# Performance work log

Measured on AMD Instinct MI355X. Metric: run time of the kernel, lower is better.

The kernel has to match this reference:

```python
import jax, jax.numpy as jnp
import numpy as np

N_NODES = 100000   # B*A = 4 * 25000 nodes after the reshape in forward()
N_EDGES = 1600000  # avg degree 16
F_IN = 2           # node_features
HID = 64           # hidden_size
K = 3              # diffusion order (hardcoded in RecurrentGCN)


def _glorot(key, shape):
    fan_in, fan_out = shape[-2], shape[-1]
    s = float(np.sqrt(6.0 / (fan_in + fan_out)))
    return jax.random.uniform(key, shape, jnp.float32, -s, s)


def setup_inputs() -> dict:
    key = jax.random.key(0)
    ks = jax.random.split(key, 12)
    x = jax.random.normal(ks[0], (4, 25000, 12, F_IN), dtype=jnp.float32)
    edge_index = jax.random.randint(ks[1], (2, N_EDGES), 0, N_NODES, dtype=jnp.int32)
    edge_weight = jax.random.uniform(ks[2], (N_EDGES,), dtype=jnp.float32)

    def cell(k, cin):
        kw = jax.random.split(k, 3)
        # 3 gates (z, r, h), each a DConv with weight [2, K, cin, HID]
        W = jnp.stack([_glorot(kw[i], (2, K, cin, HID)) for i in range(3)])
        b = jnp.zeros((3, HID), dtype=jnp.float32)
        return W, b

    enc1_W, enc1_b = cell(ks[3], F_IN + HID)
    enc2_W, enc2_b = cell(ks[4], HID + HID)
    dec1_W, dec1_b = cell(ks[5], F_IN + HID)
    dec2_W, dec2_b = cell(ks[6], HID + HID)
    lin_W = _glorot(ks[7], (HID, F_IN))
    lin_b = jnp.zeros((F_IN,), dtype=jnp.float32)
    return dict(x=x, edge_index=edge_index, edge_weight=edge_weight,
                enc1_W=enc1_W, enc1_b=enc1_b, enc2_W=enc2_W, enc2_b=enc2_b,
                dec1_W=dec1_W, dec1_b=dec1_b, dec2_W=dec2_W, dec2_b=dec2_b,
                lin_W=lin_W, lin_b=lin_b)


def _dconv(v, src, dst, do_inv, di_inv, W, b):
    # Dual-direction diffusion conv (DConv, torch_geometric_temporal), order K.
    # Normalization is applied at the node level before gather so the
    # edge-level multiply (E x C) never needs to be a stored residual.
    def pout(u):  # out[dst] += deg_out_inv[src] * u[src]
        return jax.ops.segment_sum((do_inv[:, None] * u)[src], dst, num_segments=N_NODES)

    def pin(u):   # out[src] += deg_in_inv[dst] * u[dst]
        return jax.ops.segment_sum((di_inv[:, None] * u)[dst], src, num_segments=N_NODES)

    H = v @ (W[0, 0] + W[1, 0])
    t1o, t1i = pout(v), pin(v)
    H = H + t1o @ W[0, 1] + t1i @ W[1, 1]
    t0o = t0i = v
    for k in range(2, K):  # Chebyshev-style recurrence
        t2o = 2.0 * pout(t1o) - t0o
        t2i = 2.0 * pin(t1i) - t0i
        H = H + t2o @ W[0, k] + t2i @ W[1, k]
        t0o, t1o = t1o, t2o
        t0i, t1i = t1i, t2i
    return H + b


def _dcrnn(x, h, src, dst, do_inv, di_inv, W, b):
    # GRU cell whose gates are diffusion convolutions over [x, h].
    xh = jnp.concatenate([x, h], axis=1)
    Z = jax.nn.sigmoid(_dconv(xh, src, dst, do_inv, di_inv, W[0], b[0]))
    R = jax.nn.sigmoid(_dconv(xh, src, dst, do_inv, di_inv, W[1], b[1]))
    Ht = jnp.tanh(_dconv(jnp.concatenate([x, R * h], axis=1),
                         src, dst, do_inv, di_inv, W[2], b[2]))
    return Z * h + (1.0 - Z) * Ht


def _forward(x, edge_index, edge_weight,
             enc1_W, enc1_b, enc2_W, enc2_b,
             dec1_W, dec1_b, dec2_W, dec2_b, lin_W, lin_b):
    B, A, S, Fd = x.shape
    # permute(0,1,3,2) then [..., 0] == x[:, :, 0, :]; flatten to [B*A, F]
    xs = x[:, :, 0, :].reshape(B * A, Fd)
    src, dst = edge_index[0], edge_index[1]
    deg_out = jax.ops.segment_sum(edge_weight, src, num_segments=N_NODES)
    deg_in = jax.ops.segment_sum(edge_weight, dst, num_segments=N_NODES)
    do_inv = jnp.where(deg_out > 0, 1.0 / deg_out, 0.0)
    di_inv = jnp.where(deg_in > 0, 1.0 / deg_in, 0.0)
    zeros = jnp.zeros((B * A, HID), dtype=x.dtype)
    h_enc1 = _dcrnn(xs, zeros, src, dst, do_inv, di_inv, enc1_W, enc1_b)
    h = jax.nn.relu(h_enc1)
    h_enc2 = _dcrnn(h, zeros, src, dst, do_inv, di_inv, enc2_W, enc2_b)
    h = _dcrnn(xs, h_enc1, src, dst, do_inv, di_inv, dec1_W, dec1_b)
    h = jax.nn.relu(h)
    h = _dcrnn(h, h_enc2, src, dst, do_inv, di_inv, dec2_W, dec2_b)
    return h @ lin_W + lin_b


def reference(x, edge_index, edge_weight,
              enc1_W, enc1_b, enc2_W, enc2_b,
              dec1_W, dec1_b, dec2_W, dec2_b, lin_W, lin_b):
    return _forward(x, edge_index, edge_weight,
                    enc1_W, enc1_b, enc2_W, enc2_b,
                    dec1_W, dec1_b, dec2_W, dec2_b, lin_W, lin_b)
```

## Files before the change

kernel.cpp:

```cpp
#include <hip/hip_runtime.h>

#define N_NODES 100000
#define N_EDGES 1600000

typedef _Float16 f16;
typedef _Float16 f16x8 __attribute__((ext_vector_type(8)));
typedef float f32x4 __attribute__((ext_vector_type(4)));

__device__ __forceinline__ float sigf(float x) { return 1.f / (1.f + __expf(-x)); }


__global__ void count_kernel(const int* __restrict__ src, const int* __restrict__ dst,
                             int* __restrict__ cntO, int* __restrict__ cntI,
                             int* __restrict__ slotO, int* __restrict__ slotI)
{
    int i = blockIdx.x * 256 + threadIdx.x;
    if (i >= N_EDGES) return;
    slotO[i] = atomicAdd(&cntO[dst[i]], 1);
    slotI[i] = atomicAdd(&cntI[src[i]], 1);
}

__global__ __launch_bounds__(1024) void scan2_kernel(const int* __restrict__ cntA, int* __restrict__ rpA,
                                                     const int* __restrict__ cntB, int* __restrict__ rpB,
                                                     int n)
{
    const int* cnt = blockIdx.x ? cntB : cntA;
    int* rp = blockIdx.x ? rpB : rpA;
    __shared__ int wsum[16];
    __shared__ int carry;
    int tid = threadIdx.x, lane = tid & 63, wid = tid >> 6;
    if (tid == 0) { rp[0] = 0; carry = 0; }
    __syncthreads();
    for (int base = 0; base < n; base += 1024) {
        int idx = base + tid;
        int x = (idx < n) ? cnt[idx] : 0;
        #pragma unroll
        for (int off = 1; off < 64; off <<= 1) {
            int y = __shfl_up(x, off);
            if (lane >= off) x += y;
        }
        if (lane == 63) wsum[wid] = x;
        __syncthreads();
        if (wid == 0 && lane < 16) {
            int y = wsum[lane];
            #pragma unroll
            for (int off = 1; off < 16; off <<= 1) {
                int z = __shfl_up(y, off);
                if (lane >= off) y += z;
            }
            wsum[lane] = y;
        }
        __syncthreads();
        int tot = x + (wid ? wsum[wid - 1] : 0) + carry;
        if (idx < n) rp[idx + 1] = tot;
        __syncthreads();
        if (tid == 1023) carry = tot;
        __syncthreads();
    }
}

__global__ void fill_kernel(const int* __restrict__ src, const int* __restrict__ dst,
                            const float* __restrict__ ew,
                            const int* __restrict__ rpO, const int* __restrict__ rpI,
                            const int* __restrict__ slotO, const int* __restrict__ slotI,
                            int2* __restrict__ adj2O, int2* __restrict__ adj2I)
{
    int i = blockIdx.x * 256 + threadIdx.x;
    if (i >= N_EDGES) return;
    int s = src[i], d = dst[i];
    int wb = __float_as_int(ew[i]);
    int2 eo; eo.x = s; eo.y = wb;
    adj2O[rpO[d] + slotO[i]] = eo;
    int2 ei; ei.x = d; ei.y = wb;
    adj2I[rpI[s] + slotI[i]] = ei;
}

__global__ void finalize_kernel(const int* __restrict__ rpO, const int2* __restrict__ adj2O,
                                int* __restrict__ adjO, float* __restrict__ di_inv,
                                const int* __restrict__ rpI, const int2* __restrict__ adj2I,
                                int* __restrict__ adjI, float* __restrict__ do_inv)
{
    int n = blockIdx.x * 256 + threadIdx.x;
    if (n >= N_NODES) return;
    float s = 0.f;
    for (int e = rpO[n]; e < rpO[n + 1]; ++e) {
        int2 v = adj2O[e];
        adjO[e] = v.x;
        s += __int_as_float(v.y);
    }
    di_inv[n] = (s > 0.f) ? 1.f / s : 0.f;
    float t = 0.f;
    for (int e = rpI[n]; e < rpI[n + 1]; ++e) {
        int2 v = adj2I[e];
        adjI[e] = v.x;
        t += __int_as_float(v.y);
    }
    do_inv[n] = (t > 0.f) ? 1.f / t : 0.f;
}

__global__ void prep_w(const float* __restrict__ W, int C, int SA, int PWA, int rA,
                       int gLo, int gHi, int COLS, int XS, f16* __restrict__ outw)
{
    int total = (SA + XS) * COLS * 32;
    int idx = blockIdx.x * 256 + threadIdx.x;
    if (idx >= total) return;
    int k32 = idx & 31;
    int c = (idx >> 5) % COLS;
    int s = (idx >> 5) / COLS;
    int g = (c < 64 || gHi < 0) ? gLo : gHi;
    int col = (c >= 64) ? c - 64 : c;
    int p, r;
    if (s < SA) { p = s / PWA; r = rA + (s % PWA) * 32 + k32; }
    else {
        if (k32 < 10) { p = k32 >> 1; r = k32 & 1; }
        else { outw[idx] = (f16)0.f; return; }
    }
    auto wv = [&](int d, int k) {
        return W[((((size_t)(g * 2 + d) * 3 + k) * C + r) << 6) + col];
    };
    float val;
    if (p == 0)      val = wv(0, 0) + wv(1, 0) - wv(0, 2) - wv(1, 2);
    else if (p == 1) val = wv(0, 1);
    else if (p == 2) val = 2.f * wv(0, 2);
    else if (p == 3) val = wv(1, 1);
    else             val = 2.f * wv(1, 2);
    outw[idx] = (f16)val;
}

__global__ void prep_enc1w(const float* __restrict__ W, float* __restrict__ outw)
{
    int idx = blockIdx.x * 256 + threadIdx.x;
    if (idx >= 1280) return;
    int c = idx & 127, k = idx >> 7;
    int g = (c < 64) ? 0 : 2, col = c & 63;
    int p = k >> 1, r = k & 1;
    const int C = 66;
    auto wv = [&](int d, int kk) {
        return W[((((size_t)(g * 2 + d) * 3 + kk) * C + r) << 6) + col];
    };
    float val;
    if (p == 0)      val = wv(0, 0) + wv(1, 0) - wv(0, 2) - wv(1, 2);
    else if (p == 1) val = wv(0, 1);
    else if (p == 2) val = 2.f * wv(0, 2);
    else if (p == 3) val = wv(1, 1);
    else             val = 2.f * wv(1, 2);
    outw[idx] = val;
}

__global__ void xcat_init(const float* __restrict__ x, f16* __restrict__ xcat)
{
    int i = blockIdx.x * 256 + threadIdx.x;
    if (i >= N_NODES * 32) return;
    int n = i >> 5, c = i & 31;
    float v = (c < 2) ? x[(size_t)n * 24 + c] : 0.f;
    xcat[i] = (f16)v;
}

__global__ void prop2d_kernel(const int* __restrict__ rpA, const int* __restrict__ adjA,
                              const float* __restrict__ scA, int cinA, int coutA,
                              const int* __restrict__ rpB, const int* __restrict__ adjB,
                              const float* __restrict__ scB, int cinB, int coutB,
                              f16* __restrict__ xcat)
{
    const int* rp; const int* adj; const float* sc; int cin, cout;
    if (blockIdx.y == 0) { rp = rpA; adj = adjA; sc = scA; cin = cinA; cout = coutA; }
    else                 { rp = rpB; adj = adjB; sc = scB; cin = cinB; cout = coutB; }
    int n = blockIdx.x * 256 + threadIdx.x;
    if (n >= N_NODES) return;
    int beg = rp[n], end = rp[n + 1];
    float a0 = 0.f, a1 = 0.f;
    for (int e = beg; e < end; ++e) {
        int s = adj[e];
        float w = sc[s];
        a0 += w * (float)xcat[((size_t)s << 5) + cin];
        a1 += w * (float)xcat[((size_t)s << 5) + cin + 1];
    }
    xcat[((size_t)n << 5) + cout] = (f16)a0;
    xcat[((size_t)n << 5) + cout + 1] = (f16)a1;
}

template <int LPN>
__global__ __launch_bounds__(256) void propk(
    const int* __restrict__ rpA, const int* __restrict__ adjA, const float* __restrict__ scA,
    const f16* __restrict__ uA, f16* __restrict__ oA,
    const int* __restrict__ rpB, const int* __restrict__ adjB, const float* __restrict__ scB,
    const f16* __restrict__ uB, f16* __restrict__ oB,
    int ldu, int ldo)
{
    const int* RP; const int* ADJ; const float* SC; const f16* U; f16* OUT;
    if (blockIdx.y == 0) { RP = rpA; ADJ = adjA; SC = scA; U = uA; OUT = oA; }
    else                 { RP = rpB; ADJ = adjB; SC = scB; U = uB; OUT = oB; }
    constexpr int NPB = 256 / LPN;
    int node = blockIdx.x * NPB + (threadIdx.x / LPN);
    int l = threadIdx.x % LPN;
    if (node >= N_NODES) return;
    int b = RP[node], e = RP[node + 1];
    float a[8] = {0.f, 0.f, 0.f, 0.f, 0.f, 0.f, 0.f, 0.f};
    float c[8] = {0.f, 0.f, 0.f, 0.f, 0.f, 0.f, 0.f, 0.f};
    int i = b;
    for (; i + 1 < e; i += 2) {
        int s0 = ADJ[i], s1 = ADJ[i + 1];
        float w0 = SC[s0], w1 = SC[s1];
        f16x8 u0 = *(const f16x8*)(U + (size_t)s0 * ldu + (l << 3));
        f16x8 u1 = *(const f16x8*)(U + (size_t)s1 * ldu + (l << 3));
        #pragma unroll
        for (int j = 0; j < 8; ++j) { a[j] += w0 * (float)u0[j]; c[j] += w1 * (float)u1[j]; }
    }
    if (i < e) {
        int s = ADJ[i];
        float w = SC[s];
        f16x8 u0 = *(const f16x8*)(U + (size_t)s * ldu + (l << 3));
        #pragma unroll
        for (int j = 0; j < 8; ++j) a[j] += w * (float)u0[j];
    }
    f16x8 r;
    #pragma unroll
    for (int j = 0; j < 8; ++j) r[j] = (f16)(a[j] + c[j]);
    *(f16x8*)(OUT + (size_t)node * ldo + (l << 3)) = r;
}

template <int SA, int XS, int COLS, int ACT>
__global__ __launch_bounds__(256) void mfma_gemm(
    const f16* __restrict__ uA, const f16* __restrict__ tA0, const f16* __restrict__ tA1,
    const f16* __restrict__ tA2, const f16* __restrict__ tA3,
    int lAu, int cAu, int lAt, int cAt,
    const f16* __restrict__ xcat, const f16* __restrict__ wstep,
    const f16* __restrict__ addX,
    const float* __restrict__ biasLo, const float* __restrict__ biasHi,
    f16* __restrict__ out, int os,
    const f16* __restrict__ hmul, int hs,
    f16* __restrict__ out2, const f16* __restrict__ zin)
{
    __shared__ f16 As[64][40];
    __shared__ f16 Ws[COLS][40];
    const int row0 = blockIdx.x * 64;
    const int tid = threadIdx.x;
    const int wave = tid >> 6, lane = tid & 63;
    const int lr = lane & 15, lk = lane >> 4;
    const int ka = lk << 3;
    constexpr int RT = (COLS == 128) ? 4 : 2;
    constexpr int PWA = SA / 5;
    constexpr int STEPS = SA + XS;
    f32x4 acc[RT][2] = {};
    const f16* tA[4] = { tA0, tA1, tA2, tA3 };

    #pragma unroll
    for (int s = 0; s < STEPS; ++s) {
        __syncthreads();
        {
            int r = tid >> 2, seg = tid & 3;
            int grow = row0 + r;
            const f16* srcp;
            if (s < SA) {
                int p = s / PWA, ch = s % PWA;
                const f16* base = (p == 0) ? uA : tA[p - 1];
                int ld = (p == 0) ? lAu : lAt;
                int co = (p == 0) ? cAu : cAt;
                srcp = base + (size_t)grow * ld + co + ch * 32 + (seg << 3);
            } else {
                srcp = xcat + (((size_t)grow) << 5) + (seg << 3);
            }
            int4 v = (grow < N_NODES) ? *(const int4*)srcp : make_int4(0, 0, 0, 0);
            *(int4*)&As[r][seg << 3] = v;
        }
        for (int q = tid; q < COLS * 4; q += 256) {
            int c = q >> 2, seg = q & 3;
            *(int4*)&Ws[c][seg << 3] =
                *(const int4*)(wstep + (((size_t)(s * COLS + c)) << 5) + (seg << 3));
        }
        __syncthreads();
        if (COLS == 128) {
            f16x8 b0 = *(const f16x8*)&Ws[wave * 32 + lr][ka];
            f16x8 b1 = *(const f16x8*)&Ws[wave * 32 + 16 + lr][ka];
            #pragma unroll
            for (int rt = 0; rt < RT; ++rt) {
                f16x8 a = *(const f16x8*)&As[rt * 16 + lr][ka];
                acc[rt][0] = __builtin_amdgcn_mfma_f32_16x16x32_f16(a, b0, acc[rt][0], 0, 0, 0);
                acc[rt][1] = __builtin_amdgcn_mfma_f32_16x16x32_f16(a, b1, acc[rt][1], 0, 0, 0);
            }
        } else {
            f16x8 b0 = *(const f16x8*)&Ws[(wave & 1) * 32 + lr][ka];
            f16x8 b1 = *(const f16x8*)&Ws[(wave & 1) * 32 + 16 + lr][ka];
            #pragma unroll
            for (int rt = 0; rt < RT; ++rt) {
                f16x8 a = *(const f16x8*)&As[(wave >> 1) * 32 + rt * 16 + lr][ka];
                acc[rt][0] = __builtin_amdgcn_mfma_f32_16x16x32_f16(a, b0, acc[rt][0], 0, 0, 0);
                acc[rt][1] = __builtin_amdgcn_mfma_f32_16x16x32_f16(a, b1, acc[rt][1], 0, 0, 0);
            }
        }
    }
    if constexpr (ACT == 4) {
        __shared__ float zbuf[64][65];
        float treg[RT][2][4];
        #pragma unroll
        for (int rt = 0; rt < RT; ++rt)
            #pragma unroll
            for (int ct = 0; ct < 2; ++ct) {
                int col = wave * 32 + ct * 16 + lr;
                #pragma unroll
                for (int j = 0; j < 4; ++j) {
                    int r = rt * 16 + lk * 4 + j;
                    float v = acc[rt][ct][j] + ((col < 64) ? biasLo[col] : biasHi[col - 64]);
                    if (col < 64) zbuf[r][col] = sigf(v);
                    else          treg[rt][ct][j] = tanhf(v);
                }
            }
        __syncthreads();
        #pragma unroll
        for (int rt = 0; rt < RT; ++rt)
            #pragma unroll
            for (int ct = 0; ct < 2; ++ct) {
                int col = wave * 32 + ct * 16 + lr;
                if (col < 64) continue;
                #pragma unroll
                for (int j = 0; j < 4; ++j) {
                    int r = rt * 16 + lk * 4 + j;
                    int grow = row0 + r;
                    if (grow >= N_NODES) continue;
                    float h = (1.f - zbuf[r][col - 64]) * treg[rt][ct][j];
                    out[(size_t)grow * os + (col - 64)] = (f16)h;
                }
            }
    } else if constexpr (ACT == 5) {
        #pragma unroll
        for (int rt = 0; rt < RT; ++rt)
            #pragma unroll
            for (int ct = 0; ct < 2; ++ct) {
                int col = wave * 32 + ct * 16 + lr;
                #pragma unroll
                for (int j = 0; j < 4; ++j) {
                    int grow = row0 + rt * 16 + lk * 4 + j;
                    if (grow >= N_NODES) continue;
                    float v = acc[rt][ct][j] + ((col < 64) ? biasLo[col] : biasHi[col - 64]);
                    float sg = sigf(v);
                    if (col < 64)
                        out[((size_t)grow << 6) + col] = (f16)sg;
                    else
                        out2[((size_t)grow << 6) + (col - 64)] =
                            (f16)(sg * (float)hmul[(size_t)grow * hs + (col - 64)]);
                }
            }
    } else {
        #pragma unroll
        for (int rt = 0; rt < RT; ++rt) {
            int rbase = (COLS == 128) ? rt * 16 : (wave >> 1) * 32 + rt * 16;
            #pragma unroll
            for (int ct = 0; ct < 2; ++ct) {
                int col = ((COLS == 128) ? wave * 32 : (wave & 1) * 32) + ct * 16 + lr;
                #pragma unroll
                for (int j = 0; j < 4; ++j) {
                    int grow = row0 + rbase + lk * 4 + j;
                    if (grow >= N_NODES) continue;
                    float v = acc[rt][ct][j];
                    if (addX)   v += (float)addX[((size_t)grow << 6) + col];
                    if (biasLo) v += (col < 64) ? biasLo[col] : biasHi[col - 64];
                    if (ACT == 2) v = tanhf(v);
                    else if (ACT == 6) {
                        float t = tanhf(v);
                        float z = (float)zin[((size_t)grow << 6) + col];
                        float hv = (float)hmul[(size_t)grow * hs + col];
                        v = fmaxf(z * hv + (1.f - z) * t, 0.f);
                    }
                    out[(size_t)grow * os + col] = (f16)v;
                }
            }
        }
    }
}

__global__ __launch_bounds__(256) void enc1_kernel(const f16* __restrict__ xcat,
                                                   const float* __restrict__ We1,
                                                   const float* __restrict__ b,
                                                   f16* __restrict__ c1)
{
    int node = (blockIdx.x << 2) + (threadIdx.x >> 6);
    int lane = threadIdx.x & 63;
    float az = b[lane], at = b[128 + lane];
    #pragma unroll
    for (int k = 0; k < 10; ++k) {
        float xv = (float)xcat[((size_t)node << 5) + k];
        az += xv * We1[k * 128 + lane];
        at += xv * We1[k * 128 + 64 + lane];
    }
    float z = sigf(az), t = tanhf(at);
    float h = (1.f - z) * t;
    size_t o = (size_t)node * 128 + lane;
    c1[o] = (f16)fmaxf(h, 0.f);
    c1[o + 64] = (f16)h;
}

__global__ __launch_bounds__(256) void final_kernel(const f16* __restrict__ zb, const f16* __restrict__ gT,
                                                    const f16* __restrict__ h2,
                                                    const float* __restrict__ lW, const float* __restrict__ lb,
                                                    float* __restrict__ out)
{
    int node = (blockIdx.x << 2) + (threadIdx.x >> 6);
    int lane = threadIdx.x & 63;
    size_t i = ((size_t)node << 6) + lane;
    float z = (float)zb[i];
    float d = z * (float)h2[(size_t)node * 128 + lane] + (1.f - z) * (float)gT[i];
    float s0 = d * lW[lane * 2];
    float s1 = d * lW[lane * 2 + 1];
    #pragma unroll
    for (int off = 32; off > 0; off >>= 1) {
        s0 += __shfl_down(s0, off);
        s1 += __shfl_down(s1, off);
    }
    if (lane == 0) {
        out[node * 2]     = s0 + lb[0];
        out[node * 2 + 1] = s1 + lb[1];
    }
}


extern "C" void kernel_launch(void* const* d_in, const int* in_sizes, int n_in,
                              void* d_out, int out_size, void* d_ws, size_t ws_size,
                              hipStream_t stream)
{
    (void)in_sizes; (void)n_in; (void)out_size;
    const float* x   = (const float*)d_in[0];
    const int*  eidx = (const int*)d_in[1];
    const float* ew  = (const float*)d_in[2];
    const float* e1W = (const float*)d_in[3];
    const float* e1b = (const float*)d_in[4];
    const float* e2W = (const float*)d_in[5];
    const float* e2b = (const float*)d_in[6];
    const float* d1W = (const float*)d_in[7];
    const float* d1b = (const float*)d_in[8];
    const float* d2W = (const float*)d_in[9];
    const float* d2b = (const float*)d_in[10];
    const float* lW  = (const float*)d_in[11];
    const float* lb  = (const float*)d_in[12];
    const int* src = eidx;
    const int* dst = eidx + N_EDGES;
    const int N = N_NODES, E = N_EDGES;

    char* p = (char*)d_ws;
    auto carve = [&](size_t bytes) { char* r = p; p += (bytes + 255) & ~(size_t)255; return r; };
    size_t NC = (size_t)N * 128 * 2;
    size_t NH = (size_t)N * 64 * 2;
    int*   cntO  = (int*)carve((size_t)2 * N * 4);
    int*   cntI  = cntO + N;
    int*   rpO   = (int*)carve((size_t)(N + 1) * 4);
    int*   rpI   = (int*)carve((size_t)(N + 1) * 4);
    int*   slotO = (int*)carve((size_t)E * 4);
    int*   slotI = (int*)carve((size_t)E * 4);
    char*  uni   = carve((size_t)2 * E * 8);
    int2*  adj2O = (int2*)uni;
    int2*  adj2I = (int2*)(uni + (size_t)E * 8);
    f16*   ct0   = (f16*)uni;
    f16*   ct1   = (f16*)carve(NC);
    f16*   ct2   = (f16*)carve(NC);
    f16*   ct3   = (f16*)carve(NC);
    float* do_inv = (float*)carve((size_t)N * 4);
    float* di_inv = (float*)carve((size_t)N * 4);
    f16*   xcat = (f16*)carve((size_t)N * 32 * 2);
    f16*   c1   = (f16*)carve(NC);
    f16*   c2   = (f16*)carve(NC);
    f16*   g    = (f16*)carve(NH);
    f16*   gT   = (f16*)carve(NH);
    f16*   zb   = (f16*)carve(NH);
    f16* wE2   = (f16*)carve((size_t)10 * 128 * 32 * 2);
    f16* wD1zr = (f16*)carve((size_t)11 * 128 * 32 * 2);
    f16* wD1c  = (f16*)carve((size_t)11 * 64 * 32 * 2);
    f16* wD2zr = (f16*)carve((size_t)20 * 128 * 32 * 2);
    f16* wD2cA = (f16*)carve((size_t)10 * 64 * 32 * 2);
    f16* wD2cB = (f16*)carve((size_t)10 * 64 * 32 * 2);
    float* We1 = (float*)carve((size_t)1280 * 4);

    size_t needed = (size_t)(p - (char*)d_ws);
    if (needed > ws_size) return;

    const int eg = (E + 255) / 256;
    const int ng = (N + 255) / 256;
    const int GB = 25000;

    hipMemsetAsync(cntO, 0, (size_t)2 * N * 4, stream);
    count_kernel<<<eg, 256, 0, stream>>>(src, dst, cntO, cntI, slotO, slotI);
    scan2_kernel<<<2, 1024, 0, stream>>>(cntO, rpO, cntI, rpI, N);
    fill_kernel<<<eg, 256, 0, stream>>>(src, dst, ew, rpO, rpI, slotO, slotI, adj2O, adj2I);
    int* adjO = slotO;
    int* adjI = slotI;
    finalize_kernel<<<ng, 256, 0, stream>>>(rpO, adj2O, adjO, di_inv, rpI, adj2I, adjI, do_inv);

    auto wprep = [&](const float* W, int C, int SA, int PWA, int rA,
                     int gLo, int gHi, int COLS, int XS, f16* o) {
        int total = (SA + XS) * COLS * 32;
        prep_w<<<(total + 255) / 256, 256, 0, stream>>>(W, C, SA, PWA, rA, gLo, gHi, COLS, XS, o);
    };
    wprep(e2W, 128, 10, 2, 0,  0,  2, 128, 0, wE2);
    wprep(d1W, 66,  10, 2, 2,  0,  1, 128, 1, wD1zr);
    wprep(d1W, 66,  10, 2, 2,  2, -1,  64, 1, wD1c);
    wprep(d2W, 128, 20, 4, 0,  0,  1, 128, 0, wD2zr);
    wprep(d2W, 128, 10, 2, 0,  2, -1,  64, 0, wD2cA);
    wprep(d2W, 128, 10, 2, 64, 2, -1,  64, 0, wD2cB);
    prep_enc1w<<<5, 256, 0, stream>>>(e1W, We1);

    xcat_init<<<(N * 32 + 255) / 256, 256, 0, stream>>>(x, xcat);
    dim3 ng2(ng, 2);
    prop2d_kernel<<<ng2, 256, 0, stream>>>(rpO, adjO, do_inv, 0, 2,
                                           rpI, adjI, di_inv, 0, 6, xcat);
    prop2d_kernel<<<ng2, 256, 0, stream>>>(rpO, adjO, do_inv, 2, 4,
                                           rpI, adjI, di_inv, 6, 8, xcat);

    auto props128 = [&](const f16* u) {
        dim3 pg(N / 16, 2);
        propk<16><<<pg, 256, 0, stream>>>(rpO, adjO, do_inv, u, ct0,
                                          rpI, adjI, di_inv, u, ct2, 128, 128);
        propk<16><<<pg, 256, 0, stream>>>(rpO, adjO, do_inv, ct0, ct1,
                                          rpI, adjI, di_inv, ct2, ct3, 128, 128);
    };
    auto props64 = [&](const f16* u) {
        dim3 pg(N / 32, 2);
        propk<8><<<pg, 256, 0, stream>>>(rpO, adjO, do_inv, u, ct0,
                                         rpI, adjI, di_inv, u, ct2, 64, 128);
        propk<8><<<pg, 256, 0, stream>>>(rpO, adjO, do_inv, ct0, ct1,
                                         rpI, adjI, di_inv, ct2, ct3, 128, 128);
    };
    const int gg = (N + 63) / 64;

    enc1_kernel<<<GB, 256, 0, stream>>>(xcat, We1, e1b, c1);
    props128(c1);
    mfma_gemm<10, 0, 128, 4><<<gg, 256, 0, stream>>>(
        c1, ct0, ct1, ct2, ct3, 128, 0, 128, 0, nullptr, wE2,
        nullptr, e2b, e2b + 128, c2 + 64, 128, nullptr, 0, nullptr, nullptr);
    mfma_gemm<10, 1, 128, 5><<<gg, 256, 0, stream>>>(
        c1, ct0, ct1, ct2, ct3, 128, 64, 128, 64, xcat, wD1zr,
        nullptr, d1b, d1b + 64, zb, 64, c1 + 64, 128, g, nullptr);
    props64(g);
    mfma_gemm<10, 1, 64, 6><<<gg, 256, 0, stream>>>(
        g, ct0, ct1, ct2, ct3, 64, 0, 128, 0, xcat, wD1c,
        nullptr, d1b + 128, d1b + 128, c2, 128, c1 + 64, 128, nullptr, zb);
    props128(c2);
    mfma_gemm<20, 0, 128, 5><<<gg, 256, 0, stream>>>(
        c2, ct0, ct1, ct2, ct3, 128, 0, 128, 0, nullptr, wD2zr,
        nullptr, d2b, d2b + 64, zb, 64, c2 + 64, 128, g, nullptr);
    mfma_gemm<10, 0, 64, 0><<<gg, 256, 0, stream>>>(
        c2, ct0, ct1, ct2, ct3, 128, 0, 128, 0, nullptr, wD2cA,
        nullptr, nullptr, nullptr, gT, 64, nullptr, 0, nullptr, nullptr);
    props64(g);
    mfma_gemm<10, 0, 64, 2><<<gg, 256, 0, stream>>>(
        g, ct0, ct1, ct2, ct3, 64, 0, 128, 0, nullptr, wD2cB,
        gT, d2b + 128, d2b + 128, gT, 64, nullptr, 0, nullptr, nullptr);
    final_kernel<<<GB, 256, 0, stream>>>(zb, gT, c2 + 64, lW, lb, (float*)d_out);
}
```

Before: 1.470 ms.

## Pack per-edge normalization into CSR entries and deepen GEMM K-step to 64

```diff
diff --git a/kernel.cpp b/kernel.cpp
--- a/kernel.cpp
+++ b/kernel.cpp
@@ -76,26 +76,27 @@
 }
 
 __global__ void finalize_kernel(const int* __restrict__ rpO, const int2* __restrict__ adj2O,
-                                int* __restrict__ adjO, float* __restrict__ di_inv,
+                                float* __restrict__ di_inv,
                                 const int* __restrict__ rpI, const int2* __restrict__ adj2I,
-                                int* __restrict__ adjI, float* __restrict__ do_inv)
+                                float* __restrict__ do_inv)
 {
     int n = blockIdx.x * 256 + threadIdx.x;
     if (n >= N_NODES) return;
     float s = 0.f;
-    for (int e = rpO[n]; e < rpO[n + 1]; ++e) {
-        int2 v = adj2O[e];
-        adjO[e] = v.x;
-        s += __int_as_float(v.y);
-    }
+    for (int e = rpO[n]; e < rpO[n + 1]; ++e) s += __int_as_float(adj2O[e].y);
     di_inv[n] = (s > 0.f) ? 1.f / s : 0.f;
     float t = 0.f;
-    for (int e = rpI[n]; e < rpI[n + 1]; ++e) {
-        int2 v = adj2I[e];
-        adjI[e] = v.x;
-        t += __int_as_float(v.y);
-    }
+    for (int e = rpI[n]; e < rpI[n + 1]; ++e) t += __int_as_float(adj2I[e].y);
     do_inv[n] = (t > 0.f) ? 1.f / t : 0.f;
+}
+
+__global__ void coeff_kernel(int2* __restrict__ adj2O, const float* __restrict__ do_inv,
+                             int2* __restrict__ adj2I, const float* __restrict__ di_inv)
+{
+    int i = blockIdx.x * 256 + threadIdx.x;
+    if (i >= N_EDGES) return;
+    int2 v = adj2O[i]; v.y = __float_as_int(do_inv[v.x]); adj2O[i] = v;
+    int2 w = adj2I[i]; w.y = __float_as_int(di_inv[w.x]); adj2I[i] = w;
 }
 
 __global__ void prep_w(const float* __restrict__ W, int C, int SA, int PWA, int rA,
@@ -156,24 +157,24 @@
     xcat[i] = (f16)v;
 }
 
-__global__ void prop2d_kernel(const int* __restrict__ rpA, const int* __restrict__ adjA,
-                              const float* __restrict__ scA, int cinA, int coutA,
-                              const int* __restrict__ rpB, const int* __restrict__ adjB,
-                              const float* __restrict__ scB, int cinB, int coutB,
+__global__ void prop2d_kernel(const int* __restrict__ rpA, const int2* __restrict__ adjA,
+                              int cinA, int coutA,
+                              const int* __restrict__ rpB, const int2* __restrict__ adjB,
+                              int cinB, int coutB,
                               f16* __restrict__ xcat)
 {
-    const int* rp; const int* adj; const float* sc; int cin, cout;
-    if (blockIdx.y == 0) { rp = rpA; adj = adjA; sc = scA; cin = cinA; cout = coutA; }
-    else                 { rp = rpB; adj = adjB; sc = scB; cin = cinB; cout = coutB; }
+    const int* rp; const int2* adj; int cin, cout;
+    if (blockIdx.y == 0) { rp = rpA; adj = adjA; cin = cinA; cout = coutA; }
+    else                 { rp = rpB; adj = adjB; cin = cinB; cout = coutB; }
     int n = blockIdx.x * 256 + threadIdx.x;
     if (n >= N_NODES) return;
     int beg = rp[n], end = rp[n + 1];
     float a0 = 0.f, a1 = 0.f;
     for (int e = beg; e < end; ++e) {
-        int s = adj[e];
-        float w = sc[s];
-        a0 += w * (float)xcat[((size_t)s << 5) + cin];
-        a1 += w * (float)xcat[((size_t)s << 5) + cin + 1];
+        int2 v = adj[e];
+        float w = __int_as_float(v.y);
+        a0 += w * (float)xcat[((size_t)v.x << 5) + cin];
+        a1 += w * (float)xcat[((size_t)v.x << 5) + cin + 1];
     }
     xcat[((size_t)n << 5) + cout] = (f16)a0;
     xcat[((size_t)n << 5) + cout + 1] = (f16)a1;
@@ -181,15 +182,15 @@
 
 template <int LPN>
 __global__ __launch_bounds__(256) void propk(
-    const int* __restrict__ rpA, const int* __restrict__ adjA, const float* __restrict__ scA,
+    const int* __restrict__ rpA, const int2* __restrict__ adjA,
     const f16* __restrict__ uA, f16* __restrict__ oA,
-    const int* __restrict__ rpB, const int* __restrict__ adjB, const float* __restrict__ scB,
+    const int* __restrict__ rpB, const int2* __restrict__ adjB,
     const f16* __restrict__ uB, f16* __restrict__ oB,
     int ldu, int ldo)
 {
-    const int* RP; const int* ADJ; const float* SC; const f16* U; f16* OUT;
-    if (blockIdx.y == 0) { RP = rpA; ADJ = adjA; SC = scA; U = uA; OUT = oA; }
-    else                 { RP = rpB; ADJ = adjB; SC = scB; U = uB; OUT = oB; }
+    const int* RP; const int2* ADJ; const f16* U; f16* OUT;
+    if (blockIdx.y == 0) { RP = rpA; ADJ = adjA; U = uA; OUT = oA; }
+    else                 { RP = rpB; ADJ = adjB; U = uB; OUT = oB; }
     constexpr int NPB = 256 / LPN;
     int node = blockIdx.x * NPB + (threadIdx.x / LPN);
     int l = threadIdx.x % LPN;
@@ -199,17 +200,17 @@
     float c[8] = {0.f, 0.f, 0.f, 0.f, 0.f, 0.f, 0.f, 0.f};
     int i = b;
     for (; i + 1 < e; i += 2) {
-        int s0 = ADJ[i], s1 = ADJ[i + 1];
-        float w0 = SC[s0], w1 = SC[s1];
-        f16x8 u0 = *(const f16x8*)(U + (size_t)s0 * ldu + (l << 3));
-        f16x8 u1 = *(const f16x8*)(U + (size_t)s1 * ldu + (l << 3));
+        int2 n0 = ADJ[i], n1 = ADJ[i + 1];
+        float w0 = __int_as_float(n0.y), w1 = __int_as_float(n1.y);
+        f16x8 u0 = *(const f16x8*)(U + (size_t)n0.x * ldu + (l << 3));
+        f16x8 u1 = *(const f16x8*)(U + (size_t)n1.x * ldu + (l << 3));
         #pragma unroll
         for (int j = 0; j < 8; ++j) { a[j] += w0 * (float)u0[j]; c[j] += w1 * (float)u1[j]; }
     }
     if (i < e) {
-        int s = ADJ[i];
-        float w = SC[s];
-        f16x8 u0 = *(const f16x8*)(U + (size_t)s * ldu + (l << 3));
+        int2 n0 = ADJ[i];
+        float w = __int_as_float(n0.y);
+        f16x8 u0 = *(const f16x8*)(U + (size_t)n0.x * ldu + (l << 3));
         #pragma unroll
         for (int j = 0; j < 8; ++j) a[j] += w * (float)u0[j];
     }
@@ -225,14 +226,14 @@
     const f16* __restrict__ tA2, const f16* __restrict__ tA3,
     int lAu, int cAu, int lAt, int cAt,
     const f16* __restrict__ xcat, const f16* __restrict__ wstep,
-    const f16* __restrict__ addX,
+    const f16* __restrict__ addX, int axs,
     const float* __restrict__ biasLo, const float* __restrict__ biasHi,
     f16* __restrict__ out, int os,
     const f16* __restrict__ hmul, int hs,
-    f16* __restrict__ out2, const f16* __restrict__ zin)
-{
-    __shared__ f16 As[64][40];
-    __shared__ f16 Ws[COLS][40];
+    f16* __restrict__ out2, int o2s, const f16* __restrict__ zin)
+{
+    __shared__ f16 As[64][72];
+    __shared__ f16 Ws[COLS][72];
     const int row0 = blockIdx.x * 64;
     const int tid = threadIdx.x;
     const int wave = tid >> 6, lane = tid & 63;
@@ -241,51 +242,62 @@
     constexpr int RT = (COLS == 128) ? 4 : 2;
     constexpr int PWA = SA / 5;
     constexpr int STEPS = SA + XS;
+    constexpr int NIT = (STEPS + 1) / 2;
     f32x4 acc[RT][2] = {};
     const f16* tA[4] = { tA0, tA1, tA2, tA3 };
 
     #pragma unroll
-    for (int s = 0; s < STEPS; ++s) {
-        __syncthreads();
-        {
-            int r = tid >> 2, seg = tid & 3;
-            int grow = row0 + r;
-            const f16* srcp;
-            if (s < SA) {
-                int p = s / PWA, ch = s % PWA;
-                const f16* base = (p == 0) ? uA : tA[p - 1];
-                int ld = (p == 0) ? lAu : lAt;
-                int co = (p == 0) ? cAu : cAt;
-                srcp = base + (size_t)grow * ld + co + ch * 32 + (seg << 3);
+    for (int sp = 0; sp < NIT; ++sp) {
+        const int s0 = sp * 2;
+        const int nsub = (s0 + 2 <= STEPS) ? 2 : 1;
+        __syncthreads();
+        #pragma unroll
+        for (int t = 0; t < nsub; ++t) {
+            int s = s0 + t;
+            {
+                int r = tid >> 2, seg = tid & 3;
+                int grow = row0 + r;
+                const f16* srcp;
+                if (s < SA) {
+                    int pp = s / PWA, ch = s % PWA;
+                    const f16* base = (pp == 0) ? uA : tA[pp - 1];
+                    int ld = (pp == 0) ? lAu : lAt;
+                    int co = (pp == 0) ? cAu : cAt;
+                    srcp = base + (size_t)grow * ld + co + ch * 32 + (seg << 3);
+                } else {
+                    srcp = xcat + (((size_t)grow) << 5) + (seg << 3);
+                }
+                int4 v = (grow < N_NODES) ? *(const int4*)srcp : make_int4(0, 0, 0, 0);
+                *(int4*)&As[r][t * 32 + (seg << 3)] = v;
+            }
+            for (int q = tid; q < COLS * 4; q += 256) {
+                int cc = q >> 2, sg = q & 3;
+                *(int4*)&Ws[cc][t * 32 + (sg << 3)] =
+                    *(const int4*)(wstep + (((size_t)(s * COLS + cc)) << 5) + (sg << 3));
+            }
+        }
+        __syncthreads();
+        #pragma unroll
+        for (int t = 0; t < nsub; ++t) {
+            int kb = t * 32 + ka;
+            if (COLS == 128) {
+                f16x8 b0 = *(const f16x8*)&Ws[wave * 32 + lr][kb];
+                f16x8 b1 = *(const f16x8*)&Ws[wave * 32 + 16 + lr][kb];
+                #pragma unroll
+                for (int rt = 0; rt < RT; ++rt) {
+                    f16x8 a = *(const f16x8*)&As[rt * 16 + lr][kb];
+                    acc[rt][0] = __builtin_amdgcn_mfma_f32_16x16x32_f16(a, b0, acc[rt][0], 0, 0, 0);
+                    acc[rt][1] = __builtin_amdgcn_mfma_f32_16x16x32_f16(a, b1, acc[rt][1], 0, 0, 0);
+                }
             } else {
-                srcp = xcat + (((size_t)grow) << 5) + (seg << 3);
-            }
-            int4 v = (grow < N_NODES) ? *(const int4*)srcp : make_int4(0, 0, 0, 0);
-            *(int4*)&As[r][seg << 3] = v;
-        }
-        for (int q = tid; q < COLS * 4; q += 256) {
-            int c = q >> 2, seg = q & 3;
-            *(int4*)&Ws[c][seg << 3] =
-                *(const int4*)(wstep + (((size_t)(s * COLS + c)) << 5) + (seg << 3));
-        }
-        __syncthreads();
-        if (COLS == 128) {
-            f16x8 b0 = *(const f16x8*)&Ws[wave * 32 + lr][ka];
-            f16x8 b1 = *(const f16x8*)&Ws[wave * 32 + 16 + lr][ka];
-            #pragma unroll
-            for (int rt = 0; rt < RT; ++rt) {
-                f16x8 a = *(const f16x8*)&As[rt * 16 + lr][ka];
-                acc[rt][0] = __builtin_amdgcn_mfma_f32_16x16x32_f16(a, b0, acc[rt][0], 0, 0, 0);
-                acc[rt][1] = __builtin_amdgcn_mfma_f32_16x16x32_f16(a, b1, acc[rt][1], 0, 0, 0);
-            }
-        } else {
-            f16x8 b0 = *(const f16x8*)&Ws[(wave & 1) * 32 + lr][ka];
-            f16x8 b1 = *(const f16x8*)&Ws[(wave & 1) * 32 + 16 + lr][ka];
-            #pragma unroll
-            for (int rt = 0; rt < RT; ++rt) {
-                f16x8 a = *(const f16x8*)&As[(wave >> 1) * 32 + rt * 16 + lr][ka];
-                acc[rt][0] = __builtin_amdgcn_mfma_f32_16x16x32_f16(a, b0, acc[rt][0], 0, 0, 0);
-                acc[rt][1] = __builtin_amdgcn_mfma_f32_16x16x32_f16(a, b1, acc[rt][1], 0, 0, 0);
+                f16x8 b0 = *(const f16x8*)&Ws[(wave & 1) * 32 + lr][kb];
+                f16x8 b1 = *(const f16x8*)&Ws[(wave & 1) * 32 + 16 + lr][kb];
+                #pragma unroll
+                for (int rt = 0; rt < RT; ++rt) {
+                    f16x8 a = *(const f16x8*)&As[(wave >> 1) * 32 + rt * 16 + lr][kb];
+                    acc[rt][0] = __builtin_amdgcn_mfma_f32_16x16x32_f16(a, b0, acc[rt][0], 0, 0, 0);
+                    acc[rt][1] = __builtin_amdgcn_mfma_f32_16x16x32_f16(a, b1, acc[rt][1], 0, 0, 0);
+                }
             }
         }
     }
@@ -334,9 +346,9 @@
                     float v = acc[rt][ct][j] + ((col < 64) ? biasLo[col] : biasHi[col - 64]);
                     float sg = sigf(v);
                     if (col < 64)
-                        out[((size_t)grow << 6) + col] = (f16)sg;
+                        out[(size_t)grow * os + col] = (f16)sg;
                     else
-                        out2[((size_t)grow << 6) + (col - 64)] =
+                        out2[(size_t)grow * o2s + (col - 64)] =
                             (f16)(sg * (float)hmul[(size_t)grow * hs + (col - 64)]);
                 }
             }
@@ -352,7 +364,7 @@
                     int grow = row0 + rbase + lk * 4 + j;
                     if (grow >= N_NODES) continue;
                     float v = acc[rt][ct][j];
-                    if (addX)   v += (float)addX[((size_t)grow << 6) + col];
+                    if (addX)   v += (float)addX[(size_t)grow * axs + col];
                     if (biasLo) v += (col < 64) ? biasLo[col] : biasHi[col - 64];
                     if (ACT == 2) v = tanhf(v);
                     else if (ACT == 6) {
@@ -389,16 +401,17 @@
     c1[o + 64] = (f16)h;
 }
 
-__global__ __launch_bounds__(256) void final_kernel(const f16* __restrict__ zb, const f16* __restrict__ gT,
+__global__ __launch_bounds__(256) void final_kernel(const f16* __restrict__ zb,
+                                                    const f16* __restrict__ gT,
                                                     const f16* __restrict__ h2,
                                                     const float* __restrict__ lW, const float* __restrict__ lb,
                                                     float* __restrict__ out)
 {
     int node = (blockIdx.x << 2) + (threadIdx.x >> 6);
     int lane = threadIdx.x & 63;
-    size_t i = ((size_t)node << 6) + lane;
-    float z = (float)zb[i];
-    float d = z * (float)h2[(size_t)node * 128 + lane] + (1.f - z) * (float)gT[i];
+    float z = (float)zb[((size_t)node << 6) + lane];
+    float d = z * (float)h2[(size_t)node * 128 + lane]
+            + (1.f - z) * (float)gT[(size_t)node * 128 + lane];
     float s0 = d * lW[lane * 2];
     float s1 = d * lW[lane * 2 + 1];
     #pragma unroll
@@ -438,17 +451,15 @@
     char* p = (char*)d_ws;
     auto carve = [&](size_t bytes) { char* r = p; p += (bytes + 255) & ~(size_t)255; return r; };
     size_t NC = (size_t)N * 128 * 2;
-    size_t NH = (size_t)N * 64 * 2;
     int*   cntO  = (int*)carve((size_t)2 * N * 4);
     int*   cntI  = cntO + N;
     int*   rpO   = (int*)carve((size_t)(N + 1) * 4);
     int*   rpI   = (int*)carve((size_t)(N + 1) * 4);
-    int*   slotO = (int*)carve((size_t)E * 4);
-    int*   slotI = (int*)carve((size_t)E * 4);
-    char*  uni   = carve((size_t)2 * E * 8);
-    int2*  adj2O = (int2*)uni;
-    int2*  adj2I = (int2*)(uni + (size_t)E * 8);
-    f16*   ct0   = (f16*)uni;
+    int*   slotO = (int*)carve((size_t)2 * E * 4);
+    int*   slotI = slotO + E;
+    int2*  adj2O = (int2*)carve((size_t)E * 8);
+    int2*  adj2I = (int2*)carve((size_t)E * 8);
+    f16*   ct0   = (f16*)carve(NC);
     f16*   ct1   = (f16*)carve(NC);
     f16*   ct2   = (f16*)carve(NC);
     f16*   ct3   = (f16*)carve(NC);
@@ -457,9 +468,6 @@
     f16*   xcat = (f16*)carve((size_t)N * 32 * 2);
     f16*   c1   = (f16*)carve(NC);
     f16*   c2   = (f16*)carve(NC);
-    f16*   g    = (f16*)carve(NH);
-    f16*   gT   = (f16*)carve(NH);
-    f16*   zb   = (f16*)carve(NH);
     f16* wE2   = (f16*)carve((size_t)10 * 128 * 32 * 2);
     f16* wD1zr = (f16*)carve((size_t)11 * 128 * 32 * 2);
     f16* wD1c  = (f16*)carve((size_t)11 * 64 * 32 * 2);
@@ -468,6 +476,10 @@
     f16* wD2cB = (f16*)carve((size_t)10 * 64 * 32 * 2);
     float* We1 = (float*)carve((size_t)1280 * 4);
 
+    f16* zb = (f16*)slotO;
+    f16* g1 = ct1 + 64;
+    f16* gT = ct0 + 64;
+
     size_t needed = (size_t)(p - (char*)d_ws);
     if (needed > ws_size) return;
 
@@ -479,9 +491,8 @@
     count_kernel<<<eg, 256, 0, stream>>>(src, dst, cntO, cntI, slotO, slotI);
     scan2_kernel<<<2, 1024, 0, stream>>>(cntO, rpO, cntI, rpI, N);
     fill_kernel<<<eg, 256, 0, stream>>>(src, dst, ew, rpO, rpI, slotO, slotI, adj2O, adj2I);
-    int* adjO = slotO;
-    int* adjI = slotI;
-    finalize_kernel<<<ng, 256, 0, stream>>>(rpO, adj2O, adjO, di_inv, rpI, adj2I, adjI, do_inv);
+    finalize_kernel<<<ng, 256, 0, stream>>>(rpO, adj2O, di_inv, rpI, adj2I, do_inv);
+    coeff_kernel<<<eg, 256, 0, stream>>>(adj2O, do_inv, adj2I, di_inv);
 
     auto wprep = [&](const float* W, int C, int SA, int PWA, int rA,
                      int gLo, int gHi, int COLS, int XS, f16* o) {
@@ -498,24 +509,18 @@
 
     xcat_init<<<(N * 32 + 255) / 256, 256, 0, stream>>>(x, xcat);
     dim3 ng2(ng, 2);
-    prop2d_kernel<<<ng2, 256, 0, stream>>>(rpO, adjO, do_inv, 0, 2,
-                                           rpI, adjI, di_inv, 0, 6, xcat);
-    prop2d_kernel<<<ng2, 256, 0, stream>>>(rpO, adjO, do_inv, 2, 4,
-                                           rpI, adjI, di_inv, 6, 8, xcat);
+    prop2d_kernel<<<ng2, 256, 0, stream>>>(rpO, adj2O, 0, 2, rpI, adj2I, 0, 6, xcat);
+    prop2d_kernel<<<ng2, 256, 0, stream>>>(rpO, adj2O, 2, 4, rpI, adj2I, 6, 8, xcat);
 
     auto props128 = [&](const f16* u) {
         dim3 pg(N / 16, 2);
-        propk<16><<<pg, 256, 0, stream>>>(rpO, adjO, do_inv, u, ct0,
-                                          rpI, adjI, di_inv, u, ct2, 128, 128);
-        propk<16><<<pg, 256, 0, stream>>>(rpO, adjO, do_inv, ct0, ct1,
-                                          rpI, adjI, di_inv, ct2, ct3, 128, 128);
+        propk<16><<<pg, 256, 0, stream>>>(rpO, adj2O, u, ct0, rpI, adj2I, u, ct2, 128, 128);
+        propk<16><<<pg, 256, 0, stream>>>(rpO, adj2O, ct0, ct1, rpI, adj2I, ct2, ct3, 128, 128);
     };
-    auto props64 = [&](const f16* u) {
+    auto props64 = [&](const f16* u, int ldu) {
         dim3 pg(N / 32, 2);
-        propk<8><<<pg, 256, 0, stream>>>(rpO, adjO, do_inv, u, ct0,
-                                         rpI, adjI, di_inv, u, ct2, 64, 128);
-        propk<8><<<pg, 256, 0, stream>>>(rpO, adjO, do_inv, ct0, ct1,
-                                         rpI, adjI, di_inv, ct2, ct3, 128, 128);
+        propk<8><<<pg, 256, 0, stream>>>(rpO, adj2O, u, ct0, rpI, adj2I, u, ct2, ldu, 128);
+        propk<8><<<pg, 256, 0, stream>>>(rpO, adj2O, ct0, ct1, rpI, adj2I, ct2, ct3, 128, 128);
     };
     const int gg = (N + 63) / 64;
 
@@ -523,24 +528,24 @@
     props128(c1);
     mfma_gemm<10, 0, 128, 4><<<gg, 256, 0, stream>>>(
         c1, ct0, ct1, ct2, ct3, 128, 0, 128, 0, nullptr, wE2,
-        nullptr, e2b, e2b + 128, c2 + 64, 128, nullptr, 0, nullptr, nullptr);
+        nullptr, 0, e2b, e2b + 128, c2 + 64, 128, nullptr, 0, nullptr, 0, nullptr);
     mfma_gemm<10, 1, 128, 5><<<gg, 256, 0, stream>>>(
         c1, ct0, ct1, ct2, ct3, 128, 64, 128, 64, xcat, wD1zr,
-        nullptr, d1b, d1b + 64, zb, 64, c1 + 64, 128, g, nullptr);
-    props64(g);
+        nullptr, 0, d1b, d1b + 64, zb, 64, c1 + 64, 128, g1, 128, nullptr);
+    props64(g1, 128);
     mfma_gemm<10, 1, 64, 6><<<gg, 256, 0, stream>>>(
-        g, ct0, ct1, ct2, ct3, 64, 0, 128, 0, xcat, wD1c,
-        nullptr, d1b + 128, d1b + 128, c2, 128, c1 + 64, 128, nullptr, zb);
+        g1, ct0, ct1, ct2, ct3, 128, 0, 128, 0, xcat, wD1c,
+        nullptr, 0, d1b + 128, d1b + 128, c2, 128, c1 + 64, 128, nullptr, 0, zb);
     props128(c2);
     mfma_gemm<20, 0, 128, 5><<<gg, 256, 0, stream>>>(
         c2, ct0, ct1, ct2, ct3, 128, 0, 128, 0, nullptr, wD2zr,
-        nullptr, d2b, d2b + 64, zb, 64, c2 + 64, 128, g, nullptr);
+        nullptr, 0, d2b, d2b + 64, zb, 64, c2 + 64, 128, g1, 128, nullptr);
     mfma_gemm<10, 0, 64, 0><<<gg, 256, 0, stream>>>(
         c2, ct0, ct1, ct2, ct3, 128, 0, 128, 0, nullptr, wD2cA,
-        nullptr, nullptr, nullptr, gT, 64, nullptr, 0, nullptr, nullptr);
-    props64(g);
+        nullptr, 0, nullptr, nullptr, gT, 128, nullptr, 0, nullptr, 0, nullptr);
+    props64(g1, 128);
     mfma_gemm<10, 0, 64, 2><<<gg, 256, 0, stream>>>(
-        g, ct0, ct1, ct2, ct3, 64, 0, 128, 0, nullptr, wD2cB,
-        gT, d2b + 128, d2b + 128, gT, 64, nullptr, 0, nullptr, nullptr);
+        g1, ct0, ct1, ct2, ct3, 128, 0, 128, 0, nullptr, wD2cB,
+        gT, 128, d2b + 128, d2b + 128, gT, 128, nullptr, 0, nullptr, 0, nullptr);
     final_kernel<<<GB, 256, 0, stream>>>(zb, gT, c2 + 64, lW, lb, (float*)d_out);
 }
```

Result: no change. 1.497 ms (+1.8%).
